# Kernel tuning notes

Hardware: AMD Instinct MI355X
Metric: run time of the kernel (lower is better)

## Reference

```python
import jax, jax.numpy as jnp
import numpy as np

PAD_VAL = -999
N_TYPES = 8
D_IN, D_FF, D_FFC = 512, 1024, 512
B, S = 64, 512


def setup_inputs() -> dict:
    key = jax.random.key(0)
    ks = jax.random.split(key, 6)
    sc = 0.02
    return {
        "x": jax.random.normal(ks[0], (B, S, D_IN), dtype=jnp.float32),
        "sc_types": jax.random.randint(ks[1], (B, S), 0, N_TYPES, dtype=jnp.int64),
        "W_pre": jax.random.normal(ks[2], (D_IN, D_FF), dtype=jnp.float32) * sc,
        "W_types": jax.random.normal(ks[3], (N_TYPES, D_FF, D_IN), dtype=jnp.float32) * sc,
        "W_c1": jax.random.normal(ks[4], (D_IN, D_FFC), dtype=jnp.float32) * sc,
        "W_c2": jax.random.normal(ks[5], (D_FFC, 1), dtype=jnp.float32) * sc,
    }


def reference(x, sc_types, W_pre, W_types, W_c1, W_c2):
    # flatten tokens: [B*S, d_in], [B*S]
    x = x.reshape(-1, x.shape[-1])
    t = sc_types.reshape(-1)
    # (inputs contain no PAD_VAL tokens, so the pad mask is all-True and the
    # gather x[mask] is the identity; shapes stay static)
    x_ = jax.nn.relu(x @ W_pre)                       # [N, d_ff]
    # hard type routing: select per-type MLP output for each token
    x_types = jnp.zeros_like(x)
    for i in range(N_TYPES):
        yi = jax.nn.relu(x_ @ W_types[i])             # [N, d_in]
        x_types = jnp.where((t == i)[:, None], yi, x_types)
    x = x + x_types                                    # residual combine
    h = jax.nn.relu(x @ W_c1)                          # [N, d_ffc]
    return h @ W_c2                                    # [N, 1]
```

## Files before the change

kernel.cpp:

```cpp
#include <hip/hip_runtime.h>
#include <stdint.h>

#define N_TOK 32768
#define DIN   512
#define DFF   1024
#define MPAD  33792

__device__ __forceinline__ int rotk(int k, int row) {
    return (k & ~127) + (((k & 127) + ((row & 15) << 3)) & 127);
}

typedef __attribute__((ext_vector_type(8))) short bf16x8;
typedef __attribute__((ext_vector_type(4))) float f32x4;

__device__ __forceinline__ unsigned short f2bf(float f) {
    union { float f; unsigned int u; } v; v.f = f;
    unsigned int u = v.u;
    return (unsigned short)((u + 0x7FFFu + ((u >> 16) & 1u)) >> 16);
}
__device__ __forceinline__ float bf2f(unsigned int bits) {
    union { unsigned int u; float f; } v; v.u = bits << 16; return v.f;
}
__device__ __forceinline__ unsigned int pk4_fp8(float a, float b, float c, float d) {
    int v = __builtin_amdgcn_cvt_pk_fp8_f32(a, b, 0, false);
    v = __builtin_amdgcn_cvt_pk_fp8_f32(c, d, v, true);
    return (unsigned int)v;
}
__device__ __forceinline__ unsigned char f2fp8(float a) {
    return (unsigned char)(__builtin_amdgcn_cvt_pk_fp8_f32(a, a, 0, false) & 0xFF);
}

__device__ __forceinline__ void async16(const void* g, void* l) {
    __builtin_amdgcn_global_load_lds(
        (const __attribute__((address_space(1))) void*)g,
        (__attribute__((address_space(3))) void*)l, 16, 0, 0);
}

__global__ void prep_kernel(const float* __restrict__ x,
                            unsigned short* __restrict__ Xb,
                            unsigned char* __restrict__ Xb8,
                            const int* __restrict__ types,
                            int* __restrict__ blockhist,
                            const float* __restrict__ Wp,
                            const float* __restrict__ Wt,
                            const float* __restrict__ Wc,
                            unsigned char* __restrict__ Wp8,
                            unsigned char* __restrict__ Wt8,
                            unsigned short* __restrict__ WcT,
                            int* __restrict__ perm) {
    __shared__ float tile[32][33];
    __shared__ int lc[8];
    const int b = blockIdx.x, tid = threadIdx.x;
    if (b < 16384) {
        const int i = b * 1024 + tid * 4;
        float4 v = *(const float4*)(x + i);
        ushort4 o;
        o.x = f2bf(v.x); o.y = f2bf(v.y); o.z = f2bf(v.z); o.w = f2bf(v.w);
        *(ushort4*)(Xb + i) = o;
        const int row = i >> 9;
        const int k   = i & 511;
        *(unsigned int*)(Xb8 + (size_t)row * DIN + rotk(k, row)) = pk4_fp8(v.x, v.y, v.z, v.w);
        if (b < 64) {
            if (tid < 8) lc[tid] = 0;
            __syncthreads();
            atomicAdd(&lc[types[b * 512 + tid]], 1);
            atomicAdd(&lc[types[b * 512 + 256 + tid]], 1);
            __syncthreads();
            if (tid < 8) blockhist[b * 8 + tid] = lc[tid];
        }
    } else if (b < 26624) {
        const int r = b - 16384;
        const int z = r >> 10;
        const int bx = r & 31, by = (r >> 5) & 31;
        const int tx = tid & 31, ty = tid >> 5;
        const float* s; int K, N;
        if (z == 0)      { s = Wp;                          K = 512;  N = 1024; }
        else if (z <= 8) { s = Wt + (size_t)(z-1)*DIN*DFF;  K = 1024; N = 512; }
        else             { s = Wc;                          K = 512;  N = 512; }
        const int n0 = bx * 32, k0 = by * 32;
        if (n0 >= N || k0 >= K) return;
        for (int i = ty; i < 32; i += 8)
            tile[i][tx] = s[(size_t)(k0 + i) * N + n0 + tx];
        __syncthreads();
        if (z <= 8) {
            unsigned char* d = (z == 0) ? Wp8 : (Wt8 + (size_t)(z-1)*DIN*DFF);
            const int nl = tid >> 3;
            const int k4 = (tid & 7) << 2;
            const int n  = n0 + nl;
            const int kk = k0 + k4;
            unsigned int pk = pk4_fp8(tile[k4 + 0][nl] * 64.f, tile[k4 + 1][nl] * 64.f,
                                      tile[k4 + 2][nl] * 64.f, tile[k4 + 3][nl] * 64.f);
            *(unsigned int*)(d + (size_t)n * K + rotk(kk, n)) = pk;
        } else {
            for (int i = ty; i < 32; i += 8)
                WcT[(size_t)(n0 + i) * K + k0 + tx] = f2bf(tile[tx][i]);
        }
    } else {
        perm[(b - 26624) * 256 + tid] = -1;
    }
}

__global__ void scatter_kernel(const int* __restrict__ types,
                               const int* __restrict__ blockhist,
                               int* __restrict__ perm,
                               int* __restrict__ invperm,
                               float* __restrict__ outz,
                               int* __restrict__ po_out) {
    __shared__ int tots[8], base[8], fill[8];
    const int blk = blockIdx.x;
    const int tid = threadIdx.x;
    const int i = blk * 512 + tid;
    outz[i] = 0.f;
    int pre = 0;
    if (tid < 8) {
        int total = 0;
        for (int j = 0; j < 64; j++) {
            int v = blockhist[j * 8 + tid];
            if (j < blk) pre += v;
            total += v;
        }
        tots[tid] = total;
    }
    __syncthreads();
    if (tid < 8) {
        int off = 0, pob = 0;
        #pragma unroll
        for (int t2 = 0; t2 < 8; t2++) {
            if (t2 == tid) pob = off;
            off += ((tots[t2] + 127) >> 7) << 7;
        }
        base[tid] = pob + pre;
        fill[tid] = 0;
        if (blk == 0) {
            po_out[tid] = pob;
            if (tid == 0) po_out[8] = off;
        }
    }
    __syncthreads();
    const int t = types[i];
    const int r = atomicAdd(&fill[t], 1);
    const int p = base[t] + r;
    perm[p] = i;
    invperm[i] = p;
}

__global__ __launch_bounds__(512, 2)
void gemm1_fp8_8ph(const unsigned char* __restrict__ A,
                   const unsigned char* __restrict__ B,
                   unsigned char* __restrict__ C8,
                   const int* __restrict__ invperm) {
    __shared__ unsigned char As[2][256 * 128];
    __shared__ unsigned char Bs[2][256 * 128];
    __shared__ int ptile[256];

    const int tid  = threadIdx.x;
    const int wave = tid >> 6;
    const int lane = tid & 63;
    const int quad = lane >> 4;
    const int tl   = lane & 15;

    const int lin  = blockIdx.x;
    const int sid  = (lin & 7) * 64 + (lin >> 3);
    const int m0   = (sid >> 2) * 256;
    const int n0   = (sid & 3) * 256;

    const int wm = (wave & 1) * 128;
    const int wn = (wave >> 1) * 64;

    if (tid < 256) ptile[tid] = invperm[m0 + tid];

    f32x4 acc[8][4];
    #pragma unroll
    for (int i = 0; i < 8; i++)
        #pragma unroll
        for (int j = 0; j < 4; j++)
            acc[i][j] = (f32x4){0.f, 0.f, 0.f, 0.f};

    #pragma unroll
    for (int ci = 0; ci < 8; ++ci) {
        const int c = ci * 512 + tid;
        if (ci < 4) {
            const int row = c >> 3, j = c & 7;
            async16(A + (size_t)(m0 + row) * 512 + j * 16, &As[0][c * 16]);
        } else {
            const int c2 = c - 2048;
            const int row = c2 >> 3, j = c2 & 7;
            async16(B + (size_t)(n0 + row) * 512 + j * 16, &Bs[0][c2 * 16]);
        }
    }
    asm volatile("s_waitcnt vmcnt(0)" ::: "memory");
    __builtin_amdgcn_s_barrier();
    asm volatile("" ::: "memory");

    for (int t = 0; t < 4; ++t) {
        const unsigned char* Asl = As[t & 1];
        const unsigned char* Bsl = Bs[t & 1];
        unsigned char* Asn = As[(t + 1) & 1];
        unsigned char* Bsn = Bs[(t + 1) & 1];
        const int k0n = (t + 1) * 128;
        const bool st = (t < 3);
        #pragma unroll
        for (int ph = 0; ph < 8; ++ph) {
            const int ks = ph >> 1, mh = ph & 1;
            const int o = (ks * 32 + quad * 8 + tl * 8) & 127;
            long af[4], bfr[4];
            #pragma unroll
            for (int mt = 0; mt < 4; ++mt)
                af[mt] = *(const long*)(Asl + (wm + mh * 64 + mt * 16 + tl) * 128 + o);
            #pragma unroll
            for (int nt = 0; nt < 4; ++nt)
                bfr[nt] = *(const long*)(Bsl + (wn + nt * 16 + tl) * 128 + o);
            if (st && ph < 4) {
                #pragma unroll
                for (int u = 0; u < 2; ++u) {
                    const int cidx = ph * 2 + u;
                    const int c = cidx * 512 + tid;
                    if (cidx < 4) {
                        const int row = c >> 3, j = c & 7;
                        async16(A + (size_t)(m0 + row) * 512 + k0n + j * 16, Asn + c * 16);
                    } else {
                        const int c2 = c - 2048;
                        const int row = c2 >> 3, j = c2 & 7;
                        async16(B + (size_t)(n0 + row) * 512 + k0n + j * 16, Bsn + c2 * 16);
                    }
                }
            }
            __builtin_amdgcn_s_barrier();
            asm volatile("" ::: "memory");
            __builtin_amdgcn_s_setprio(1);
            #pragma unroll
            for (int mt = 0; mt < 4; ++mt)
                #pragma unroll
                for (int nt = 0; nt < 4; ++nt)
                    acc[mh * 4 + mt][nt] = __builtin_amdgcn_mfma_f32_16x16x32_fp8_fp8(
                        bfr[nt], af[mt], acc[mh * 4 + mt][nt], 0, 0, 0);
            __builtin_amdgcn_s_setprio(0);
            if (ph == 7) asm volatile("s_waitcnt vmcnt(0)" ::: "memory");
            __builtin_amdgcn_s_barrier();
            asm volatile("" ::: "memory");
        }
    }

    #pragma unroll
    for (int mh = 0; mh < 2; ++mh)
        #pragma unroll
        for (int mt = 0; mt < 4; ++mt) {
            const int p = ptile[wm + mh * 64 + mt * 16 + tl];
            const size_t rowbase = (size_t)p * DFF;
            const int prot = (p & 15) << 3;
            #pragma unroll
            for (int nt = 0; nt < 4; ++nt) {
                const int off = wn + nt * 16 + quad * 4;
                unsigned int pk = pk4_fp8(fmaxf(acc[mh * 4 + mt][nt][0], 0.f) * 0.125f,
                                          fmaxf(acc[mh * 4 + mt][nt][1], 0.f) * 0.125f,
                                          fmaxf(acc[mh * 4 + mt][nt][2], 0.f) * 0.125f,
                                          fmaxf(acc[mh * 4 + mt][nt][3], 0.f) * 0.125f);
                const int phys = (off & ~127) + (((off & 127) + prot) & 127);
                *(unsigned int*)(C8 + rowbase + n0 + phys) = pk;
            }
        }
}

template <int MODE>
__global__ __launch_bounds__(256, 4)
void gemm_fp8_kernel(const unsigned char* __restrict__ A,
                     const unsigned char* __restrict__ B,
                     void* __restrict__ Cout,
                     const unsigned short* __restrict__ xres,
                     const int* __restrict__ pmap,
                     const int* __restrict__ po,
                     int K, int ldA) {
    __shared__ unsigned char As[128 * 128];
    __shared__ unsigned char Bs[128 * 128];
    __shared__ int ptile[128];

    const int tid  = threadIdx.x;
    const int wave = tid >> 6;
    const int lane = tid & 63;
    const int quad = lane >> 4;
    const int tl   = lane & 15;
    int m0, n0;
    if constexpr (MODE == 1) {
        const int sid = (blockIdx.x & 7) * 132 + (blockIdx.x >> 3);
        m0 = (sid >> 2) * 128;
        n0 = (sid & 3) * 128;
    } else {
        m0 = blockIdx.y * 128;
        n0 = blockIdx.x * 128;
    }
    const int wm = (wave & 1) * 64;
    const int wn = (wave >> 1) * 64;

    const unsigned char* Bp = B;
    if constexpr (MODE == 1) {
        if (m0 >= po[8]) return;
        int bsel = 0;
        #pragma unroll
        for (int i = 1; i < 8; i++) bsel += (m0 >= po[i]) ? 1 : 0;
        Bp = B + (size_t)bsel * (DIN * DFF);
    }
    if (tid < 128) ptile[tid] = pmap[m0 + tid];

    f32x4 acc[4][4];
    #pragma unroll
    for (int i = 0; i < 4; i++)
        #pragma unroll
        for (int j = 0; j < 4; j++)
            acc[i][j] = (f32x4){0.f, 0.f, 0.f, 0.f};

    for (int k0 = 0; k0 < K; k0 += 128) {
        __syncthreads();
        #pragma unroll
        for (int i = 0; i < 4; i++) {
            const int c   = (i * 4 + wave) * 64 + lane;
            const int row = c >> 3;
            const int j   = c & 7;
            async16(A + (size_t)(m0 + row) * ldA + k0 + j * 16, (char*)As + (size_t)c * 16);
        }
        #pragma unroll
        for (int i = 0; i < 4; i++) {
            const int c   = (i * 4 + wave) * 64 + lane;
            const int row = c >> 3;
            const int j   = c & 7;
            async16(Bp + (size_t)(n0 + row) * K + k0 + j * 16, (char*)Bs + (size_t)c * 16);
        }
        __syncthreads();

        #pragma unroll
        for (int ks = 0; ks < 4; ks++) {
            long af[4], bfr[4];
            const int o = (ks * 32 + quad * 8 + tl * 8) & 127;
            #pragma unroll
            for (int t = 0; t < 4; t++)
                af[t] = *(const long*)(As + (wm + t * 16 + tl) * 128 + o);
            #pragma unroll
            for (int t = 0; t < 4; t++)
                bfr[t] = *(const long*)(Bs + (wn + t * 16 + tl) * 128 + o);
            #pragma unroll
            for (int mt = 0; mt < 4; mt++)
                #pragma unroll
                for (int nt = 0; nt < 4; nt++)
                    acc[mt][nt] = __builtin_amdgcn_mfma_f32_16x16x32_fp8_fp8(
                        bfr[nt], af[mt], acc[mt][nt], 0, 0, 0);
        }
    }

    if constexpr (MODE == 0) {
        unsigned char* C8 = (unsigned char*)Cout;
        #pragma unroll
        for (int mt = 0; mt < 4; mt++) {
            const int p = ptile[wm + mt * 16 + tl];
            const size_t rowbase = (size_t)p * DFF;
            const int prot = (p & 15) << 3;
            #pragma unroll
            for (int nt = 0; nt < 4; nt++) {
                const int off = wn + nt * 16 + quad * 4;
                unsigned int pk = pk4_fp8(fmaxf(acc[mt][nt][0], 0.f) * 0.125f,
                                          fmaxf(acc[mt][nt][1], 0.f) * 0.125f,
                                          fmaxf(acc[mt][nt][2], 0.f) * 0.125f,
                                          fmaxf(acc[mt][nt][3], 0.f) * 0.125f);
                const int phys = (off & ~127) + (((off & 127) + prot) & 127);
                *(unsigned int*)(C8 + rowbase + n0 + phys) = pk;
            }
        }
    } else {
        unsigned short* Cb = (unsigned short*)Cout;
        int toks[4];
        #pragma unroll
        for (int mt = 0; mt < 4; mt++) toks[mt] = ptile[wm + mt * 16 + tl];
        ushort4 rv[4][4];
        #pragma unroll
        for (int mt = 0; mt < 4; mt++) {
            if (toks[mt] < 0) continue;
            const size_t rowbase = (size_t)toks[mt] * DIN;
            #pragma unroll
            for (int nt = 0; nt < 4; nt++)
                rv[mt][nt] = *(const ushort4*)(xres + rowbase + n0 + wn + nt * 16 + quad * 4);
        }
        #pragma unroll
        for (int mt = 0; mt < 4; mt++) {
            if (toks[mt] < 0) continue;
            const size_t rowbase = (size_t)toks[mt] * DIN;
            #pragma unroll
            for (int nt = 0; nt < 4; nt++) {
                const int ncol = n0 + wn + nt * 16 + quad * 4;
                ushort4 o;
                o.x = f2bf(bf2f(rv[mt][nt].x) + fmaxf(acc[mt][nt][0], 0.f) * 0.001953125f);
                o.y = f2bf(bf2f(rv[mt][nt].y) + fmaxf(acc[mt][nt][1], 0.f) * 0.001953125f);
                o.z = f2bf(bf2f(rv[mt][nt].z) + fmaxf(acc[mt][nt][2], 0.f) * 0.001953125f);
                o.w = f2bf(bf2f(rv[mt][nt].w) + fmaxf(acc[mt][nt][3], 0.f) * 0.001953125f);
                *(ushort4*)(Cb + rowbase + ncol) = o;
            }
        }
    }
}

__global__ __launch_bounds__(512, 4)
void gemm3_kernel(const unsigned short* __restrict__ A,
                  const unsigned short* __restrict__ B,
                  const float* __restrict__ w2,
                  float* __restrict__ outp,
                  int K, int ldA) {
    __shared__ unsigned short As[128 * 64];
    __shared__ unsigned short Bs[256 * 64];

    const int tid  = threadIdx.x;
    const int wave = tid >> 6;
    const int lane = tid & 63;
    const int quad = lane >> 4;
    const int tl   = lane & 15;
    const int sid = (blockIdx.x & 7) * 64 + (blockIdx.x >> 3);
    const int m0 = (sid >> 1) * 128;
    const int n0 = (sid & 1) * 256;
    const int wm = (wave & 1) * 64;
    const int wn = (wave >> 1) * 64;

    f32x4 acc[4][4];
    #pragma unroll
    for (int i = 0; i < 4; i++)
        #pragma unroll
        for (int j = 0; j < 4; j++)
            acc[i][j] = (f32x4){0.f, 0.f, 0.f, 0.f};

    for (int k0 = 0; k0 < K; k0 += 64) {
        __syncthreads();
        #pragma unroll
        for (int i = 0; i < 2; i++) {
            const int c   = (i * 8 + wave) * 64 + lane;
            const int row = c >> 3;
            const int gj  = (c & 7) ^ (row & 7);
            async16(A + (size_t)(m0 + row) * ldA + k0 + gj * 8, (char*)As + (size_t)c * 16);
        }
        #pragma unroll
        for (int i = 0; i < 4; i++) {
            const int c   = (i * 8 + wave) * 64 + lane;
            const int row = c >> 3;
            const int gj  = (c & 7) ^ (row & 7);
            async16(B + (size_t)(n0 + row) * K + k0 + gj * 8, (char*)Bs + (size_t)c * 16);
        }
        __syncthreads();

        #pragma unroll
        for (int ks = 0; ks < 2; ks++) {
            bf16x8 af[4], bfr[4];
            const int jc = ks * 4 + quad;
            #pragma unroll
            for (int t = 0; t < 4; t++) {
                const int r = wm + t * 16 + tl;
                af[t] = *(const bf16x8*)(As + (r * 8 + (jc ^ (r & 7))) * 8);
            }
            #pragma unroll
            for (int t = 0; t < 4; t++) {
                const int r = wn + t * 16 + tl;
                bfr[t] = *(const bf16x8*)(Bs + (r * 8 + (jc ^ (r & 7))) * 8);
            }
            #pragma unroll
            for (int mt = 0; mt < 4; mt++)
                #pragma unroll
                for (int nt = 0; nt < 4; nt++)
                    acc[mt][nt] = __builtin_amdgcn_mfma_f32_16x16x32_bf16(
                        bfr[nt], af[mt], acc[mt][nt], 0, 0, 0);
        }
    }

    float4 w2v[4];
    #pragma unroll
    for (int nt = 0; nt < 4; nt++)
        w2v[nt] = *(const float4*)(w2 + n0 + wn + nt * 16 + quad * 4);
    #pragma unroll
    for (int mt = 0; mt < 4; mt++) {
        float s = 0.f;
        #pragma unroll
        for (int nt = 0; nt < 4; nt++) {
            s += fmaxf(acc[mt][nt][0], 0.f) * w2v[nt].x;
            s += fmaxf(acc[mt][nt][1], 0.f) * w2v[nt].y;
            s += fmaxf(acc[mt][nt][2], 0.f) * w2v[nt].z;
            s += fmaxf(acc[mt][nt][3], 0.f) * w2v[nt].w;
        }
        s += __shfl_down(s, 32);
        s += __shfl_down(s, 16);
        if (lane < 16) atomicAdd(&outp[m0 + wm + mt * 16 + lane], s);
    }
}

extern "C" void kernel_launch(void* const* d_in, const int* in_sizes, int n_in,
                              void* d_out, int out_size, void* d_ws, size_t ws_size,
                              hipStream_t stream) {
    const float* x      = (const float*)d_in[0];
    const int*   types  = (const int*)d_in[1];
    const float* W_pre  = (const float*)d_in[2];
    const float* W_types= (const float*)d_in[3];
    const float* W_c1   = (const float*)d_in[4];
    const float* W_c2   = (const float*)d_in[5];
    float* out = (float*)d_out;

    char* ws = (char*)d_ws;
    unsigned short* Xb  = (unsigned short*)(ws);
    unsigned char*  Xff8= (unsigned char*)(ws + 33554432ull);
    unsigned char*  Xb8 = (unsigned char*)(ws + 68157440ull);
    unsigned char*  Wp8 = (unsigned char*)(ws + 84934656ull);
    unsigned char*  Wt8 = (unsigned char*)(ws + 85458944ull);
    unsigned short* WcT = (unsigned short*)(ws + 89653248ull);
    int* perm           = (int*)(ws + 90177536ull);
    int* invperm        = (int*)(ws + 90312704ull);
    int* po             = (int*)(ws + 90443776ull);
    int* blockhist      = po + 16;

    prep_kernel<<<26756, 256, 0, stream>>>(x, Xb, Xb8, types, blockhist,
                                           W_pre, W_types, W_c1, Wp8, Wt8, WcT, perm);
    scatter_kernel<<<64, 512, 0, stream>>>(types, blockhist, perm, invperm, out, po);
    gemm1_fp8_8ph<<<512, 512, 0, stream>>>(Xb8, Wp8, Xff8, invperm);
    gemm_fp8_kernel<1><<<1056, 256, 0, stream>>>(
        Xff8, Wt8, Xb, Xb, perm, po, 1024, 1024);
    gemm3_kernel<<<512, 512, 0, stream>>>(
        Xb, WcT, W_c2, out, 512, 512);
}
```

Baseline: 232.7 us.

## Double-buffer LDS in grouped FP8 expert GEMM with two-stage async prefetch

Replaces the templated single-buffer FP8 GEMM used for the per-type expert stage with a dedicated kernel that keeps two LDS stages. It prefetches tile k+2 while computing tile k, using vmcnt waits and raw barriers. It also raises wave priority around the MFMA block and hardcodes K=1024. The aim is to overlap global-to-LDS loads with matrix math. The cost is double the LDS use (about 64KB per block), with launch bounds lowered to 2 blocks per SM, which reduces occupancy.

```diff
diff --git a/kernel.cpp b/kernel.cpp
--- a/kernel.cpp
+++ b/kernel.cpp
@@ -261,17 +261,15 @@
         }
 }
 
-template <int MODE>
-__global__ __launch_bounds__(256, 4)
-void gemm_fp8_kernel(const unsigned char* __restrict__ A,
-                     const unsigned char* __restrict__ B,
-                     void* __restrict__ Cout,
-                     const unsigned short* __restrict__ xres,
-                     const int* __restrict__ pmap,
-                     const int* __restrict__ po,
-                     int K, int ldA) {
-    __shared__ unsigned char As[128 * 128];
-    __shared__ unsigned char Bs[128 * 128];
+__global__ __launch_bounds__(256, 2)
+void gemm2_fp8_dbuf(const unsigned char* __restrict__ A,
+                    const unsigned char* __restrict__ B,
+                    unsigned short* __restrict__ Cb,
+                    const unsigned short* __restrict__ xres,
+                    const int* __restrict__ perm,
+                    const int* __restrict__ po) {
+    __shared__ __align__(16) unsigned char As[2][128 * 128];
+    __shared__ __align__(16) unsigned char Bs[2][128 * 128];
     __shared__ int ptile[128];
 
     const int tid  = threadIdx.x;
@@ -279,27 +277,19 @@
     const int lane = tid & 63;
     const int quad = lane >> 4;
     const int tl   = lane & 15;
-    int m0, n0;
-    if constexpr (MODE == 1) {
-        const int sid = (blockIdx.x & 7) * 132 + (blockIdx.x >> 3);
-        m0 = (sid >> 2) * 128;
-        n0 = (sid & 3) * 128;
-    } else {
-        m0 = blockIdx.y * 128;
-        n0 = blockIdx.x * 128;
-    }
+    const int sid = (blockIdx.x & 7) * 132 + (blockIdx.x >> 3);
+    const int m0 = (sid >> 2) * 128;
+    const int n0 = (sid & 3) * 128;
     const int wm = (wave & 1) * 64;
     const int wn = (wave >> 1) * 64;
 
-    const unsigned char* Bp = B;
-    if constexpr (MODE == 1) {
-        if (m0 >= po[8]) return;
-        int bsel = 0;
-        #pragma unroll
-        for (int i = 1; i < 8; i++) bsel += (m0 >= po[i]) ? 1 : 0;
-        Bp = B + (size_t)bsel * (DIN * DFF);
-    }
-    if (tid < 128) ptile[tid] = pmap[m0 + tid];
+    if (m0 >= po[8]) return;
+    int bsel = 0;
+    #pragma unroll
+    for (int i = 1; i < 8; i++) bsel += (m0 >= po[i]) ? 1 : 0;
+    const unsigned char* Bp = B + (size_t)bsel * (DIN * DFF);
+
+    if (tid < 128) ptile[tid] = perm[m0 + tid];
 
     f32x4 acc[4][4];
     #pragma unroll
@@ -308,89 +298,87 @@
         for (int j = 0; j < 4; j++)
             acc[i][j] = (f32x4){0.f, 0.f, 0.f, 0.f};
 
-    for (int k0 = 0; k0 < K; k0 += 128) {
-        __syncthreads();
+    auto stage = [&](int kt, int s) {
+        const int k0 = kt * 128;
         #pragma unroll
         for (int i = 0; i < 4; i++) {
-            const int c   = (i * 4 + wave) * 64 + lane;
-            const int row = c >> 3;
-            const int j   = c & 7;
-            async16(A + (size_t)(m0 + row) * ldA + k0 + j * 16, (char*)As + (size_t)c * 16);
+            const int c = (i * 4 + wave) * 64 + lane;
+            const int row = c >> 3, j = c & 7;
+            async16(A + (size_t)(m0 + row) * 1024 + k0 + j * 16, &As[s][c * 16]);
         }
         #pragma unroll
         for (int i = 0; i < 4; i++) {
-            const int c   = (i * 4 + wave) * 64 + lane;
-            const int row = c >> 3;
-            const int j   = c & 7;
-            async16(Bp + (size_t)(n0 + row) * K + k0 + j * 16, (char*)Bs + (size_t)c * 16);
-        }
-        __syncthreads();
-
+            const int c = (i * 4 + wave) * 64 + lane;
+            const int row = c >> 3, j = c & 7;
+            async16(Bp + (size_t)(n0 + row) * 1024 + k0 + j * 16, &Bs[s][c * 16]);
+        }
+    };
+
+    stage(0, 0);
+    stage(1, 1);
+    asm volatile("s_waitcnt vmcnt(8) lgkmcnt(0)" ::: "memory");
+    __builtin_amdgcn_s_barrier();
+    asm volatile("" ::: "memory");
+
+    for (int t = 0; t < 8; ++t) {
+        const unsigned char* Asl = As[t & 1];
+        const unsigned char* Bsl = Bs[t & 1];
         #pragma unroll
         for (int ks = 0; ks < 4; ks++) {
             long af[4], bfr[4];
             const int o = (ks * 32 + quad * 8 + tl * 8) & 127;
             #pragma unroll
-            for (int t = 0; t < 4; t++)
-                af[t] = *(const long*)(As + (wm + t * 16 + tl) * 128 + o);
-            #pragma unroll
-            for (int t = 0; t < 4; t++)
-                bfr[t] = *(const long*)(Bs + (wn + t * 16 + tl) * 128 + o);
+            for (int mt = 0; mt < 4; mt++)
+                af[mt] = *(const long*)(Asl + (wm + mt * 16 + tl) * 128 + o);
+            #pragma unroll
+            for (int nt = 0; nt < 4; nt++)
+                bfr[nt] = *(const long*)(Bsl + (wn + nt * 16 + tl) * 128 + o);
+            __builtin_amdgcn_s_setprio(1);
             #pragma unroll
             for (int mt = 0; mt < 4; mt++)
                 #pragma unroll
                 for (int nt = 0; nt < 4; nt++)
                     acc[mt][nt] = __builtin_amdgcn_mfma_f32_16x16x32_fp8_fp8(
                         bfr[nt], af[mt], acc[mt][nt], 0, 0, 0);
-        }
-    }
-
-    if constexpr (MODE == 0) {
-        unsigned char* C8 = (unsigned char*)Cout;
-        #pragma unroll
-        for (int mt = 0; mt < 4; mt++) {
-            const int p = ptile[wm + mt * 16 + tl];
-            const size_t rowbase = (size_t)p * DFF;
-            const int prot = (p & 15) << 3;
-            #pragma unroll
-            for (int nt = 0; nt < 4; nt++) {
-                const int off = wn + nt * 16 + quad * 4;
-                unsigned int pk = pk4_fp8(fmaxf(acc[mt][nt][0], 0.f) * 0.125f,
-                                          fmaxf(acc[mt][nt][1], 0.f) * 0.125f,
-                                          fmaxf(acc[mt][nt][2], 0.f) * 0.125f,
-                                          fmaxf(acc[mt][nt][3], 0.f) * 0.125f);
-                const int phys = (off & ~127) + (((off & 127) + prot) & 127);
-                *(unsigned int*)(C8 + rowbase + n0 + phys) = pk;
-            }
-        }
-    } else {
-        unsigned short* Cb = (unsigned short*)Cout;
-        int toks[4];
-        #pragma unroll
-        for (int mt = 0; mt < 4; mt++) toks[mt] = ptile[wm + mt * 16 + tl];
-        ushort4 rv[4][4];
-        #pragma unroll
-        for (int mt = 0; mt < 4; mt++) {
-            if (toks[mt] < 0) continue;
-            const size_t rowbase = (size_t)toks[mt] * DIN;
-            #pragma unroll
-            for (int nt = 0; nt < 4; nt++)
-                rv[mt][nt] = *(const ushort4*)(xres + rowbase + n0 + wn + nt * 16 + quad * 4);
-        }
-        #pragma unroll
-        for (int mt = 0; mt < 4; mt++) {
-            if (toks[mt] < 0) continue;
-            const size_t rowbase = (size_t)toks[mt] * DIN;
-            #pragma unroll
-            for (int nt = 0; nt < 4; nt++) {
-                const int ncol = n0 + wn + nt * 16 + quad * 4;
-                ushort4 o;
-                o.x = f2bf(bf2f(rv[mt][nt].x) + fmaxf(acc[mt][nt][0], 0.f) * 0.001953125f);
-                o.y = f2bf(bf2f(rv[mt][nt].y) + fmaxf(acc[mt][nt][1], 0.f) * 0.001953125f);
-                o.z = f2bf(bf2f(rv[mt][nt].z) + fmaxf(acc[mt][nt][2], 0.f) * 0.001953125f);
-                o.w = f2bf(bf2f(rv[mt][nt].w) + fmaxf(acc[mt][nt][3], 0.f) * 0.001953125f);
-                *(ushort4*)(Cb + rowbase + ncol) = o;
-            }
+            __builtin_amdgcn_s_setprio(0);
+        }
+        __builtin_amdgcn_s_barrier();
+        asm volatile("" ::: "memory");
+        if (t + 2 < 8) {
+            stage(t + 2, t & 1);
+            asm volatile("s_waitcnt vmcnt(8)" ::: "memory");
+        } else {
+            asm volatile("s_waitcnt vmcnt(0)" ::: "memory");
+        }
+        __builtin_amdgcn_s_barrier();
+        asm volatile("" ::: "memory");
+    }
+
+    int toks[4];
+    #pragma unroll
+    for (int mt = 0; mt < 4; mt++) toks[mt] = ptile[wm + mt * 16 + tl];
+    ushort4 rv[4][4];
+    #pragma unroll
+    for (int mt = 0; mt < 4; mt++) {
+        if (toks[mt] < 0) continue;
+        const size_t rowbase = (size_t)toks[mt] * DIN;
+        #pragma unroll
+        for (int nt = 0; nt < 4; nt++)
+            rv[mt][nt] = *(const ushort4*)(xres + rowbase + n0 + wn + nt * 16 + quad * 4);
+    }
+    #pragma unroll
+    for (int mt = 0; mt < 4; mt++) {
+        if (toks[mt] < 0) continue;
+        const size_t rowbase = (size_t)toks[mt] * DIN;
+        #pragma unroll
+        for (int nt = 0; nt < 4; nt++) {
+            const int ncol = n0 + wn + nt * 16 + quad * 4;
+            ushort4 o;
+            o.x = f2bf(bf2f(rv[mt][nt].x) + fmaxf(acc[mt][nt][0], 0.f) * 0.001953125f);
+            o.y = f2bf(bf2f(rv[mt][nt].y) + fmaxf(acc[mt][nt][1], 0.f) * 0.001953125f);
+            o.z = f2bf(bf2f(rv[mt][nt].z) + fmaxf(acc[mt][nt][2], 0.f) * 0.001953125f);
+            o.w = f2bf(bf2f(rv[mt][nt].w) + fmaxf(acc[mt][nt][3], 0.f) * 0.001953125f);
+            *(ushort4*)(Cb + rowbase + ncol) = o;
         }
     }
 }
@@ -510,8 +498,7 @@
                                            W_pre, W_types, W_c1, Wp8, Wt8, WcT, perm);
     scatter_kernel<<<64, 512, 0, stream>>>(types, blockhist, perm, invperm, out, po);
     gemm1_fp8_8ph<<<512, 512, 0, stream>>>(Xb8, Wp8, Xff8, invperm);
-    gemm_fp8_kernel<1><<<1056, 256, 0, stream>>>(
-        Xff8, Wt8, Xb, Xb, perm, po, 1024, 1024);
+    gemm2_fp8_dbuf<<<1056, 256, 0, stream>>>(Xff8, Wt8, Xb, Xb, perm, po);
     gemm3_kernel<<<512, 512, 0, stream>>>(
         Xb, WcT, W_c2, out, 512, 512);
 }
```

Result: slower. 238.3 us (+2.4%).

## Pipeline grouped GEMM2 with 256-row tiles and triple-buffered async ring

Applied to the files above, without the earlier changes.

The per-type grouped GEMM (gemm2) becomes a 512-thread kernel with 256x128 tiles and a three-slot shared-memory ring, so loads for k-tile t+2 are issued while MFMAs run on tile t. Tiles are now laid out per type segment with a row limit, which removes the per-tile type lookup and cuts padding waste. GEMM1 goes back from the 8-phase double-buffered 256x256 kernel to a simpler 128x128 non-pipelined kernel. The risk is that GEMM1 slows down and that the larger shared-memory footprint of gemm2 lowers occupancy.

```diff
diff --git a/kernel.cpp b/kernel.cpp
--- a/kernel.cpp
+++ b/kernel.cpp
@@ -144,162 +144,130 @@
     invperm[i] = p;
 }
 
-__global__ __launch_bounds__(512, 2)
-void gemm1_fp8_8ph(const unsigned char* __restrict__ A,
-                   const unsigned char* __restrict__ B,
-                   unsigned char* __restrict__ C8,
-                   const int* __restrict__ invperm) {
-    __shared__ unsigned char As[2][256 * 128];
-    __shared__ unsigned char Bs[2][256 * 128];
-    __shared__ int ptile[256];
+__global__ __launch_bounds__(256, 4)
+void gemm1_fp8_kernel(const unsigned char* __restrict__ A,
+                      const unsigned char* __restrict__ B,
+                      unsigned char* __restrict__ C8,
+                      const int* __restrict__ invperm) {
+    __shared__ unsigned char As[128 * 128];
+    __shared__ unsigned char Bs[128 * 128];
+    __shared__ int ptile[128];
 
     const int tid  = threadIdx.x;
     const int wave = tid >> 6;
     const int lane = tid & 63;
     const int quad = lane >> 4;
     const int tl   = lane & 15;
-
-    const int lin  = blockIdx.x;
-    const int sid  = (lin & 7) * 64 + (lin >> 3);
-    const int m0   = (sid >> 2) * 256;
-    const int n0   = (sid & 3) * 256;
-
-    const int wm = (wave & 1) * 128;
+    const int m0 = blockIdx.y * 128;
+    const int n0 = blockIdx.x * 128;
+    const int wm = (wave & 1) * 64;
     const int wn = (wave >> 1) * 64;
 
-    if (tid < 256) ptile[tid] = invperm[m0 + tid];
-
-    f32x4 acc[8][4];
-    #pragma unroll
-    for (int i = 0; i < 8; i++)
+    if (tid < 128) ptile[tid] = invperm[m0 + tid];
+
+    f32x4 acc[4][4];
+    #pragma unroll
+    for (int i = 0; i < 4; i++)
         #pragma unroll
         for (int j = 0; j < 4; j++)
             acc[i][j] = (f32x4){0.f, 0.f, 0.f, 0.f};
 
-    #pragma unroll
-    for (int ci = 0; ci < 8; ++ci) {
-        const int c = ci * 512 + tid;
-        if (ci < 4) {
-            const int row = c >> 3, j = c & 7;
-            async16(A + (size_t)(m0 + row) * 512 + j * 16, &As[0][c * 16]);
-        } else {
-            const int c2 = c - 2048;
-            const int row = c2 >> 3, j = c2 & 7;
-            async16(B + (size_t)(n0 + row) * 512 + j * 16, &Bs[0][c2 * 16]);
-        }
-    }
-    asm volatile("s_waitcnt vmcnt(0)" ::: "memory");
-    __builtin_amdgcn_s_barrier();
-    asm volatile("" ::: "memory");
-
-    for (int t = 0; t < 4; ++t) {
-        const unsigned char* Asl = As[t & 1];
-        const unsigned char* Bsl = Bs[t & 1];
-        unsigned char* Asn = As[(t + 1) & 1];
-        unsigned char* Bsn = Bs[(t + 1) & 1];
-        const int k0n = (t + 1) * 128;
-        const bool st = (t < 3);
-        #pragma unroll
-        for (int ph = 0; ph < 8; ++ph) {
-            const int ks = ph >> 1, mh = ph & 1;
+    for (int k0 = 0; k0 < 512; k0 += 128) {
+        __syncthreads();
+        #pragma unroll
+        for (int i = 0; i < 4; i++) {
+            const int c   = (i * 4 + wave) * 64 + lane;
+            const int row = c >> 3;
+            const int j   = c & 7;
+            async16(A + (size_t)(m0 + row) * 512 + k0 + j * 16, (char*)As + (size_t)c * 16);
+        }
+        #pragma unroll
+        for (int i = 0; i < 4; i++) {
+            const int c   = (i * 4 + wave) * 64 + lane;
+            const int row = c >> 3;
+            const int j   = c & 7;
+            async16(B + (size_t)(n0 + row) * 512 + k0 + j * 16, (char*)Bs + (size_t)c * 16);
+        }
+        __syncthreads();
+
+        #pragma unroll
+        for (int ks = 0; ks < 4; ks++) {
+            long af[4], bfr[4];
             const int o = (ks * 32 + quad * 8 + tl * 8) & 127;
-            long af[4], bfr[4];
-            #pragma unroll
-            for (int mt = 0; mt < 4; ++mt)
-                af[mt] = *(const long*)(Asl + (wm + mh * 64 + mt * 16 + tl) * 128 + o);
-            #pragma unroll
-            for (int nt = 0; nt < 4; ++nt)
-                bfr[nt] = *(const long*)(Bsl + (wn + nt * 16 + tl) * 128 + o);
-            if (st && ph < 4) {
+            #pragma unroll
+            for (int t = 0; t < 4; t++)
+                af[t] = *(const long*)(As + (wm + t * 16 + tl) * 128 + o);
+            #pragma unroll
+            for (int t = 0; t < 4; t++)
+                bfr[t] = *(const long*)(Bs + (wn + t * 16 + tl) * 128 + o);
+            #pragma unroll
+            for (int mt = 0; mt < 4; mt++)
                 #pragma unroll
-                for (int u = 0; u < 2; ++u) {
-                    const int cidx = ph * 2 + u;
-                    const int c = cidx * 512 + tid;
-                    if (cidx < 4) {
-                        const int row = c >> 3, j = c & 7;
-                        async16(A + (size_t)(m0 + row) * 512 + k0n + j * 16, Asn + c * 16);
-                    } else {
-                        const int c2 = c - 2048;
-                        const int row = c2 >> 3, j = c2 & 7;
-                        async16(B + (size_t)(n0 + row) * 512 + k0n + j * 16, Bsn + c2 * 16);
-                    }
-                }
-            }
-            __builtin_amdgcn_s_barrier();
-            asm volatile("" ::: "memory");
-            __builtin_amdgcn_s_setprio(1);
-            #pragma unroll
-            for (int mt = 0; mt < 4; ++mt)
-                #pragma unroll
-                for (int nt = 0; nt < 4; ++nt)
-                    acc[mh * 4 + mt][nt] = __builtin_amdgcn_mfma_f32_16x16x32_fp8_fp8(
-                        bfr[nt], af[mt], acc[mh * 4 + mt][nt], 0, 0, 0);
-            __builtin_amdgcn_s_setprio(0);
-            if (ph == 7) asm volatile("s_waitcnt vmcnt(0)" ::: "memory");
-            __builtin_amdgcn_s_barrier();
-            asm volatile("" ::: "memory");
-        }
-    }
-
-    #pragma unroll
-    for (int mh = 0; mh < 2; ++mh)
-        #pragma unroll
-        for (int mt = 0; mt < 4; ++mt) {
-            const int p = ptile[wm + mh * 64 + mt * 16 + tl];
-            const size_t rowbase = (size_t)p * DFF;
-            const int prot = (p & 15) << 3;
-            #pragma unroll
-            for (int nt = 0; nt < 4; ++nt) {
-                const int off = wn + nt * 16 + quad * 4;
-                unsigned int pk = pk4_fp8(fmaxf(acc[mh * 4 + mt][nt][0], 0.f) * 0.125f,
-                                          fmaxf(acc[mh * 4 + mt][nt][1], 0.f) * 0.125f,
-                                          fmaxf(acc[mh * 4 + mt][nt][2], 0.f) * 0.125f,
-                                          fmaxf(acc[mh * 4 + mt][nt][3], 0.f) * 0.125f);
-                const int phys = (off & ~127) + (((off & 127) + prot) & 127);
-                *(unsigned int*)(C8 + rowbase + n0 + phys) = pk;
-            }
-        }
-}
-
-template <int MODE>
-__global__ __launch_bounds__(256, 4)
-void gemm_fp8_kernel(const unsigned char* __restrict__ A,
-                     const unsigned char* __restrict__ B,
-                     void* __restrict__ Cout,
-                     const unsigned short* __restrict__ xres,
-                     const int* __restrict__ pmap,
-                     const int* __restrict__ po,
-                     int K, int ldA) {
-    __shared__ unsigned char As[128 * 128];
-    __shared__ unsigned char Bs[128 * 128];
-    __shared__ int ptile[128];
+                for (int nt = 0; nt < 4; nt++)
+                    acc[mt][nt] = __builtin_amdgcn_mfma_f32_16x16x32_fp8_fp8(
+                        bfr[nt], af[mt], acc[mt][nt], 0, 0, 0);
+        }
+    }
+
+    #pragma unroll
+    for (int mt = 0; mt < 4; mt++) {
+        const int p = ptile[wm + mt * 16 + tl];
+        const size_t rowbase = (size_t)p * DFF;
+        const int prot = (p & 15) << 3;
+        #pragma unroll
+        for (int nt = 0; nt < 4; nt++) {
+            const int off = wn + nt * 16 + quad * 4;
+            unsigned int pk = pk4_fp8(fmaxf(acc[mt][nt][0], 0.f) * 0.125f,
+                                      fmaxf(acc[mt][nt][1], 0.f) * 0.125f,
+                                      fmaxf(acc[mt][nt][2], 0.f) * 0.125f,
+                                      fmaxf(acc[mt][nt][3], 0.f) * 0.125f);
+            const int phys = (off & ~127) + (((off & 127) + prot) & 127);
+            *(unsigned int*)(C8 + rowbase + n0 + phys) = pk;
+        }
+    }
+}
+
+__global__ __launch_bounds__(512, 2)
+void gemm2_fp8_ring(const unsigned char* __restrict__ A,
+                    const unsigned char* __restrict__ B,
+                    unsigned short* __restrict__ Cb,
+                    const unsigned short* __restrict__ xres,
+                    const int* __restrict__ perm,
+                    const int* __restrict__ po) {
+    __shared__ __align__(16) unsigned char As[3][256 * 128];
+    __shared__ __align__(16) unsigned char Bs[3][128 * 128];
+    __shared__ int ptile[256];
 
     const int tid  = threadIdx.x;
     const int wave = tid >> 6;
     const int lane = tid & 63;
     const int quad = lane >> 4;
     const int tl   = lane & 15;
-    int m0, n0;
-    if constexpr (MODE == 1) {
-        const int sid = (blockIdx.x & 7) * 132 + (blockIdx.x >> 3);
-        m0 = (sid >> 2) * 128;
-        n0 = (sid & 3) * 128;
-    } else {
-        m0 = blockIdx.y * 128;
-        n0 = blockIdx.x * 128;
-    }
-    const int wm = (wave & 1) * 64;
-    const int wn = (wave >> 1) * 64;
-
-    const unsigned char* Bp = B;
-    if constexpr (MODE == 1) {
-        if (m0 >= po[8]) return;
-        int bsel = 0;
-        #pragma unroll
-        for (int i = 1; i < 8; i++) bsel += (m0 >= po[i]) ? 1 : 0;
-        Bp = B + (size_t)bsel * (DIN * DFF);
-    }
-    if (tid < 128) ptile[tid] = pmap[m0 + tid];
+    const int sid = (blockIdx.x & 7) * 68 + (blockIdx.x >> 3);
+    const int tau = sid >> 2;
+    const int n0  = (sid & 3) * 128;
+    const int wm  = (wave >> 1) * 64;
+    const int wn  = (wave & 1) * 64;
+
+    int pox[9];
+    #pragma unroll
+    for (int i = 0; i < 9; i++) pox[i] = po[i];
+    int m0 = -1, lim = 0, bsel = 0, acc0 = 0;
+    #pragma unroll
+    for (int bb = 0; bb < 8; ++bb) {
+        const int len = pox[bb + 1] - pox[bb];
+        const int ntl = (len + 255) >> 8;
+        if (tau >= acc0 && tau < acc0 + ntl) {
+            m0 = pox[bb] + (tau - acc0) * 256;
+            lim = pox[bb + 1];
+            bsel = bb;
+        }
+        acc0 += ntl;
+    }
+    if (m0 < 0) return;
+    const unsigned char* Bp = B + (size_t)bsel * (DIN * DFF);
+
+    if (tid < 256) ptile[tid] = perm[m0 + tid];
 
     f32x4 acc[4][4];
     #pragma unroll
@@ -308,89 +276,97 @@
         for (int j = 0; j < 4; j++)
             acc[i][j] = (f32x4){0.f, 0.f, 0.f, 0.f};
 
-    for (int k0 = 0; k0 < K; k0 += 128) {
-        __syncthreads();
-        #pragma unroll
-        for (int i = 0; i < 4; i++) {
-            const int c   = (i * 4 + wave) * 64 + lane;
-            const int row = c >> 3;
-            const int j   = c & 7;
-            async16(A + (size_t)(m0 + row) * ldA + k0 + j * 16, (char*)As + (size_t)c * 16);
-        }
-        #pragma unroll
-        for (int i = 0; i < 4; i++) {
-            const int c   = (i * 4 + wave) * 64 + lane;
-            const int row = c >> 3;
-            const int j   = c & 7;
-            async16(Bp + (size_t)(n0 + row) * K + k0 + j * 16, (char*)Bs + (size_t)c * 16);
-        }
-        __syncthreads();
-
-        #pragma unroll
-        for (int ks = 0; ks < 4; ks++) {
+    auto unit = [&](int kt, int s, int u) {
+        const int k0 = kt * 128;
+        if (u < 4) {
+            const int c = u * 512 + tid;
+            const int row = c >> 3, j = c & 7;
+            async16(A + (size_t)(m0 + row) * 1024 + k0 + j * 16, &As[s][c * 16]);
+        } else {
+            const int c = (u - 4) * 512 + tid;
+            const int row = c >> 3, j = c & 7;
+            async16(Bp + (size_t)(n0 + row) * 1024 + k0 + j * 16, &Bs[s][c * 16]);
+        }
+    };
+
+    #pragma unroll
+    for (int u = 0; u < 6; ++u) unit(0, 0, u);
+    #pragma unroll
+    for (int u = 0; u < 6; ++u) unit(1, 1, u);
+    asm volatile("s_waitcnt vmcnt(6)" ::: "memory");
+    __builtin_amdgcn_s_barrier();
+    asm volatile("" ::: "memory");
+
+    #pragma unroll
+    for (int t = 0; t < 8; ++t) {
+        const int slot = t % 3;
+        const unsigned char* Asl = &As[slot][0];
+        const unsigned char* Bsl = &Bs[slot][0];
+        const int pslot = (t + 2) % 3;
+        #pragma unroll
+        for (int ks = 0; ks < 4; ++ks) {
             long af[4], bfr[4];
             const int o = (ks * 32 + quad * 8 + tl * 8) & 127;
             #pragma unroll
-            for (int t = 0; t < 4; t++)
-                af[t] = *(const long*)(As + (wm + t * 16 + tl) * 128 + o);
-            #pragma unroll
-            for (int t = 0; t < 4; t++)
-                bfr[t] = *(const long*)(Bs + (wn + t * 16 + tl) * 128 + o);
+            for (int mt = 0; mt < 4; mt++)
+                af[mt] = *(const long*)(Asl + (wm + mt * 16 + tl) * 128 + o);
+            #pragma unroll
+            for (int nt = 0; nt < 4; nt++)
+                bfr[nt] = *(const long*)(Bsl + (wn + nt * 16 + tl) * 128 + o);
+            if (t + 2 < 8) {
+                if (ks == 0) { unit(t + 2, pslot, 0); unit(t + 2, pslot, 1); }
+                else if (ks == 1) { unit(t + 2, pslot, 2); unit(t + 2, pslot, 3); }
+                else if (ks == 2) { unit(t + 2, pslot, 4); }
+                else { unit(t + 2, pslot, 5); }
+            }
+            __builtin_amdgcn_s_barrier();
+            asm volatile("s_waitcnt lgkmcnt(0)" ::: "memory");
+            __builtin_amdgcn_sched_barrier(0);
+            __builtin_amdgcn_s_setprio(1);
             #pragma unroll
             for (int mt = 0; mt < 4; mt++)
                 #pragma unroll
                 for (int nt = 0; nt < 4; nt++)
                     acc[mt][nt] = __builtin_amdgcn_mfma_f32_16x16x32_fp8_fp8(
                         bfr[nt], af[mt], acc[mt][nt], 0, 0, 0);
-        }
-    }
-
-    if constexpr (MODE == 0) {
-        unsigned char* C8 = (unsigned char*)Cout;
-        #pragma unroll
-        for (int mt = 0; mt < 4; mt++) {
-            const int p = ptile[wm + mt * 16 + tl];
-            const size_t rowbase = (size_t)p * DFF;
-            const int prot = (p & 15) << 3;
-            #pragma unroll
-            for (int nt = 0; nt < 4; nt++) {
-                const int off = wn + nt * 16 + quad * 4;
-                unsigned int pk = pk4_fp8(fmaxf(acc[mt][nt][0], 0.f) * 0.125f,
-                                          fmaxf(acc[mt][nt][1], 0.f) * 0.125f,
-                                          fmaxf(acc[mt][nt][2], 0.f) * 0.125f,
-                                          fmaxf(acc[mt][nt][3], 0.f) * 0.125f);
-                const int phys = (off & ~127) + (((off & 127) + prot) & 127);
-                *(unsigned int*)(C8 + rowbase + n0 + phys) = pk;
+            __builtin_amdgcn_s_setprio(0);
+            if (ks == 3 && t < 7) {
+                if (t + 2 < 8) asm volatile("s_waitcnt vmcnt(6)" ::: "memory");
+                else           asm volatile("s_waitcnt vmcnt(0)" ::: "memory");
             }
-        }
-    } else {
-        unsigned short* Cb = (unsigned short*)Cout;
-        int toks[4];
-        #pragma unroll
-        for (int mt = 0; mt < 4; mt++) toks[mt] = ptile[wm + mt * 16 + tl];
-        ushort4 rv[4][4];
-        #pragma unroll
-        for (int mt = 0; mt < 4; mt++) {
-            if (toks[mt] < 0) continue;
-            const size_t rowbase = (size_t)toks[mt] * DIN;
-            #pragma unroll
-            for (int nt = 0; nt < 4; nt++)
-                rv[mt][nt] = *(const ushort4*)(xres + rowbase + n0 + wn + nt * 16 + quad * 4);
-        }
-        #pragma unroll
-        for (int mt = 0; mt < 4; mt++) {
-            if (toks[mt] < 0) continue;
-            const size_t rowbase = (size_t)toks[mt] * DIN;
-            #pragma unroll
-            for (int nt = 0; nt < 4; nt++) {
-                const int ncol = n0 + wn + nt * 16 + quad * 4;
-                ushort4 o;
-                o.x = f2bf(bf2f(rv[mt][nt].x) + fmaxf(acc[mt][nt][0], 0.f) * 0.001953125f);
-                o.y = f2bf(bf2f(rv[mt][nt].y) + fmaxf(acc[mt][nt][1], 0.f) * 0.001953125f);
-                o.z = f2bf(bf2f(rv[mt][nt].z) + fmaxf(acc[mt][nt][2], 0.f) * 0.001953125f);
-                o.w = f2bf(bf2f(rv[mt][nt].w) + fmaxf(acc[mt][nt][3], 0.f) * 0.001953125f);
-                *(ushort4*)(Cb + rowbase + ncol) = o;
-            }
+            __builtin_amdgcn_s_barrier();
+            asm volatile("" ::: "memory");
+        }
+    }
+
+    int toks[4];
+    #pragma unroll
+    for (int mt = 0; mt < 4; mt++) {
+        const int p = m0 + wm + mt * 16 + tl;
+        toks[mt] = (p < lim) ? ptile[wm + mt * 16 + tl] : -1;
+    }
+    ushort4 rv[4][4];
+    #pragma unroll
+    for (int mt = 0; mt < 4; mt++) {
+        if (toks[mt] < 0) continue;
+        const size_t rowbase = (size_t)toks[mt] * DIN;
+        #pragma unroll
+        for (int nt = 0; nt < 4; nt++)
+            rv[mt][nt] = *(const ushort4*)(xres + rowbase + n0 + wn + nt * 16 + quad * 4);
+    }
+    #pragma unroll
+    for (int mt = 0; mt < 4; mt++) {
+        if (toks[mt] < 0) continue;
+        const size_t rowbase = (size_t)toks[mt] * DIN;
+        #pragma unroll
+        for (int nt = 0; nt < 4; nt++) {
+            const int ncol = n0 + wn + nt * 16 + quad * 4;
+            ushort4 o;
+            o.x = f2bf(bf2f(rv[mt][nt].x) + fmaxf(acc[mt][nt][0], 0.f) * 0.001953125f);
+            o.y = f2bf(bf2f(rv[mt][nt].y) + fmaxf(acc[mt][nt][1], 0.f) * 0.001953125f);
+            o.z = f2bf(bf2f(rv[mt][nt].z) + fmaxf(acc[mt][nt][2], 0.f) * 0.001953125f);
+            o.w = f2bf(bf2f(rv[mt][nt].w) + fmaxf(acc[mt][nt][3], 0.f) * 0.001953125f);
+            *(ushort4*)(Cb + rowbase + ncol) = o;
         }
     }
 }
@@ -509,9 +485,9 @@
     prep_kernel<<<26756, 256, 0, stream>>>(x, Xb, Xb8, types, blockhist,
                                            W_pre, W_types, W_c1, Wp8, Wt8, WcT, perm);
     scatter_kernel<<<64, 512, 0, stream>>>(types, blockhist, perm, invperm, out, po);
-    gemm1_fp8_8ph<<<512, 512, 0, stream>>>(Xb8, Wp8, Xff8, invperm);
-    gemm_fp8_kernel<1><<<1056, 256, 0, stream>>>(
-        Xff8, Wt8, Xb, Xb, perm, po, 1024, 1024);
+    gemm1_fp8_kernel<<<dim3(DFF / 128, N_TOK / 128), 256, 0, stream>>>(
+        Xb8, Wp8, Xff8, invperm);
+    gemm2_fp8_ring<<<544, 512, 0, stream>>>(Xff8, Wt8, Xb, Xb, perm, po);
     gemm3_kernel<<<512, 512, 0, stream>>>(
         Xb, WcT, W_c2, out, 512, 512);
 }
```

New measurement: 248.4 us. 6.8% more time.
